# Performance work log

Hardware: AMD Instinct MI355X
Metric: run time of the kernel (lower is better)

Reference implementation:

```python
import jax, jax.numpy as jnp
import numpy as np
from jax import lax

NUM_CHANNELS = 64
DILATION_DEPTH = 9
NUM_REPEAT = 2
KERNEL_SIZE = 3
DILATIONS = [2 ** d for d in range(DILATION_DEPTH)] * NUM_REPEAT  # 18 layers
B, T = 4, 32768


def causal_conv1d(x, w, b, dilation):
    # x: [B, Cin, T], w: [Cout, Cin, K], b: [Cout]
    # left-pad by (K-1)*dilation -> causal, output length T
    pad = (w.shape[-1] - 1) * dilation
    out = lax.conv_general_dilated(
        x, w, window_strides=(1,), padding=[(pad, 0)],
        rhs_dilation=(dilation,), dimension_numbers=("NCH", "OIH", "NCH"))
    return out + b[None, :, None]


def setup_inputs() -> dict:
    key = jax.random.key(0)
    ks = jax.random.split(key, 9)
    L, C = len(DILATIONS), NUM_CHANNELS
    s = 0.05
    return {
        "x": jax.random.normal(ks[0], (B, 1, T), dtype=jnp.float32),
        "in_w": jax.random.normal(ks[1], (C, 1, 1), dtype=jnp.float32) * s,
        "in_b": jax.random.normal(ks[2], (C,), dtype=jnp.float32) * s,
        "hid_w": jax.random.normal(ks[3], (L, 2 * C, C, KERNEL_SIZE), dtype=jnp.float32) * s,
        "hid_b": jax.random.normal(ks[4], (L, 2 * C), dtype=jnp.float32) * s,
        "res_w": jax.random.normal(ks[5], (L, C, C, 1), dtype=jnp.float32) * s,
        "res_b": jax.random.normal(ks[6], (L, C), dtype=jnp.float32) * s,
        "mix_w": jax.random.normal(ks[7], (1, L * C, 1), dtype=jnp.float32) * s,
        "mix_b": jax.random.normal(ks[8], (1,), dtype=jnp.float32) * s,
    }


def reference(x, in_w, in_b, hid_w, hid_b, res_w, res_b, mix_w, mix_b):
    C = NUM_CHANNELS
    out = causal_conv1d(x, in_w, in_b, 1)  # [B, C, T]
    skips = []
    for i, d in enumerate(DILATIONS):
        inp = out
        h = causal_conv1d(inp, hid_w[i], hid_b[i], d)  # [B, 2C, T]
        gated = jnp.tanh(h[:, :C]) * jax.nn.sigmoid(h[:, C:])  # [B, C, T]
        skips.append(gated)
        out = causal_conv1d(gated, res_w[i], res_b[i], 1) + inp
    skip_cat = jnp.concatenate(skips, axis=1)  # [B, L*C, T]
    return causal_conv1d(skip_cat, mix_w, mix_b, 1)  # [B, 1, T]
```

## Files before the change

### kernel.cpp

```cpp
#include <hip/hip_runtime.h>
#include <math.h>

#define T_LEN 32768
#define NB 4
#define NC 64
#define NL 18

typedef __attribute__((ext_vector_type(8))) short s16x8;
typedef __attribute__((ext_vector_type(4))) float f32x4;
#define MFMA_F16 __builtin_amdgcn_mfma_f32_16x16x32_f16

#define BAR_LGKM()                                                   \
    do {                                                             \
        asm volatile("s_waitcnt lgkmcnt(0)" ::: "memory");           \
        __builtin_amdgcn_s_barrier();                                \
        __builtin_amdgcn_sched_barrier(0);                           \
    } while (0)
#define BAR_VM(N)                                                    \
    do {                                                             \
        asm volatile("s_waitcnt vmcnt(%0) lgkmcnt(0)" ::             \
                         "i"(N) : "memory");                         \
        __builtin_amdgcn_s_barrier();                                \
        __builtin_amdgcn_sched_barrier(0);                           \
    } while (0)

__device__ inline unsigned short f2h(float f) {
    _Float16 h = (_Float16)f;
    return __builtin_bit_cast(unsigned short, h);
}
__device__ inline unsigned pack_h2(float a, float b) {
    return (unsigned)f2h(a) | ((unsigned)f2h(b) << 16);
}
__device__ inline float h2f(unsigned short u) {
    return (float)__builtin_bit_cast(_Float16, u);
}
__device__ inline float fast_sigmoid(float x) {
    return __builtin_amdgcn_rcpf(1.f + __expf(-x));
}
__device__ inline float fast_tanh(float x) {
    return 1.f - 2.f * __builtin_amdgcn_rcpf(1.f + __expf(2.f * x));
}

__global__ void prep_kernel(const float* __restrict__ hid_w,
                            const float* __restrict__ res_w,
                            const float* __restrict__ mix_b,
                            unsigned short* __restrict__ Wh,
                            unsigned short* __restrict__ Wr,
                            float* __restrict__ out,
                            float* __restrict__ zerobuf) {
    const int nW1 = NL * 128 * 192;
    const int nW2 = NL * 64 * 64;
    const int nOut = NB * T_LEN;
    const int total = nW1 + nW2 + nOut + 32;
    for (int gid = blockIdx.x * blockDim.x + threadIdx.x; gid < total;
         gid += gridDim.x * blockDim.x) {
        if (gid < nW1) {
            int K = gid % 192;
            int co = (gid / 192) & 127;
            int i = gid / (192 * 128);
            int kt = K >> 6, ci = K & 63;
            Wh[gid] = f2h(hid_w[((i * 128 + co) * 64 + ci) * 3 + kt]);
        } else if (gid < nW1 + nW2) {
            int q = gid - nW1;
            int c = q & 63, co = (q >> 6) & 63, i = q >> 12;
            Wr[q] = f2h(res_w[(i * 64 + co) * 64 + c]);
        } else if (gid < nW1 + nW2 + nOut) {
            out[gid - (nW1 + nW2)] = mix_b[0];
        } else {
            zerobuf[gid - (nW1 + nW2 + nOut)] = 0.f;
        }
    }
}

template <int DIL, bool FIRST, bool LAST>
__launch_bounds__(256, 4)
__global__ void layer_kernel(const unsigned short* __restrict__ actH,
                             unsigned short* __restrict__ outH,
                             const unsigned short* __restrict__ Wh,
                             const float* __restrict__ hb,
                             const unsigned short* __restrict__ Wr,
                             const float* __restrict__ rb,
                             const float* __restrict__ mw,
                             float* __restrict__ skip,
                             const float* __restrict__ zerobuf,
                             const float* __restrict__ x,
                             const float* __restrict__ in_w,
                             const float* __restrict__ in_b) {
    constexpr bool UNI = (DIL < 64);
    constexpr int R = UNI ? (64 + 2 * DIL) : 192;
    constexpr int SLOTS = R * 8;
    constexpr int JMAX = (SLOTS + 255) / 256;
    constexpr int GS_BASE = (UNI ? 128 : 0) * 128;
    constexpr int OUT_BASE = (UNI ? 0 : 64) * 128;
    constexpr int REG = 24576;

    __shared__ uint4 Xs[2 * 1536];
    __shared__ float Sk[256];
    char* lds = (char*)Xs;

    const int tid = threadIdx.x;
    const int w = tid >> 6;
    const int l = tid & 63;
    const int lo = l & 15;
    const int hi = l >> 4;
    const int blk = blockIdx.x;
    const int tile = (blk & 7) * 64 + (blk >> 3);
    const int t0 = tile * 64;
    const int m0 = 16 * w;
    const int c0 = m0 + 4 * hi;

    const float* xB0 = x;

    s16x8 AH[2][6];
    s16x8 AR[2];
#pragma unroll
    for (int mt = 0; mt < 2; mt++) {
        const unsigned short* wp = Wh + (size_t)(m0 + 64 * mt + lo) * 192;
#pragma unroll
        for (int s = 0; s < 6; s++)
            AH[mt][s] = *(const s16x8*)(wp + 32 * s + 8 * hi);
    }
    if (!LAST) {
#pragma unroll
        for (int s = 0; s < 2; s++)
            AR[s] = *(const s16x8*)(Wr + (size_t)(m0 + lo) * 64 + 32 * s + 8 * hi);
    }
    float bA[4], bB[4], rbv[4];
#pragma unroll
    for (int r = 0; r < 4; r++) {
        bA[r] = hb[c0 + r];
        bB[r] = hb[64 + c0 + r];
        rbv[r] = LAST ? 0.f : rb[c0 + r];
    }
    const float4 mw4 = *(const float4*)(mw + c0);

    auto stage_async = [&](int bb, char* X) {
        const unsigned short* aB = actH + (size_t)bb * T_LEN * NC;
#pragma unroll
        for (int jj = 0; jj < JMAX; jj++) {
            int s = (w * JMAX + jj) * 64 + l;
            const void* src;
            if (s >= SLOTS) {
                src = (const void*)(zerobuf + (s & 7) * 4);
            } else {
                int row = s >> 3, ch = s & 7;
                int chunk = ch ^ (row & 7);
                int tg = t0 + (UNI ? (row - 2 * DIL)
                                   : (((row >> 6) - 2) * DIL + (row & 63)));
                src = (tg >= 0)
                          ? (const void*)(aB + (size_t)tg * 64 + chunk * 8)
                          : (const void*)(zerobuf + chunk * 4);
            }
            __builtin_amdgcn_global_load_lds(
                (const __attribute__((address_space(1))) unsigned int*)src,
                (__attribute__((address_space(3))) unsigned int*)(X +
                                                        (w * JMAX + jj) * 1024),
                16, 0, 0);
        }
    };
    auto stage_first = [&](int bb, char* X) {
        const float* xB = xB0 + (size_t)bb * T_LEN;
#pragma unroll
        for (int jj = 0; jj < JMAX; jj++) {
            int p = jj * 256 + tid;
            if (p < SLOTS) {
                int row = p >> 3, ch = p & 7;
                int tg = t0 + row - 2 * DIL;
                unsigned uu[4] = {0u, 0u, 0u, 0u};
                if (tg >= 0) {
                    float a = xB[tg];
#pragma unroll
                    for (int e = 0; e < 4; e++) {
                        float v0 = a * in_w[ch * 8 + 2 * e] + in_b[ch * 8 + 2 * e];
                        float v1 = a * in_w[ch * 8 + 2 * e + 1] + in_b[ch * 8 + 2 * e + 1];
                        uu[e] = pack_h2(v0, v1);
                    }
                }
                int byte = (row * 128 + ch * 16) ^ ((row & 7) << 4);
                *(uint4*)(X + byte) = make_uint4(uu[0], uu[1], uu[2], uu[3]);
            }
        }
    };

    if (FIRST) stage_first(0, lds);
    else       stage_async(0, lds);

#pragma unroll
    for (int j = 0; j < NB; j++) {
        char* X = lds + (j & 1) * REG;
        const int b = j;

        if (j + 1 < NB) {
            if (FIRST) stage_first(j + 1, lds + ((j + 1) & 1) * REG);
            else       stage_async(j + 1, lds + ((j + 1) & 1) * REG);
        }

        if (FIRST)          BAR_LGKM();
        else if (j + 1 < NB) BAR_VM(JMAX);
        else                 BAR_VM(0);

        f32x4 acc[2][4];
#pragma unroll
        for (int mt = 0; mt < 2; mt++)
#pragma unroll
            for (int nt = 0; nt < 4; nt++)
                acc[mt][nt] = (f32x4){0.f, 0.f, 0.f, 0.f};
#pragma unroll
        for (int s = 0; s < 6; s++) {
            const int tap = s >> 1, half = s & 1;
#pragma unroll
            for (int nt = 0; nt < 4; nt++) {
                int t = 16 * nt + lo;
                int row = UNI ? (t + tap * DIL) : (tap * 64 + t);
                int byte = (row * 128 + half * 64 + hi * 16) ^ ((row & 7) << 4);
                s16x8 bx = __builtin_bit_cast(s16x8, *(const uint4*)(X + byte));
                acc[0][nt] = MFMA_F16(AH[0][s], bx, acc[0][nt], 0, 0, 0);
                acc[1][nt] = MFMA_F16(AH[1][s], bx, acc[1][nt], 0, 0, 0);
            }
        }

        float4 inp[4];
        if (!LAST) {
#pragma unroll
            for (int nt = 0; nt < 4; nt++) {
                int t = 16 * nt + lo;
                int rowI = UNI ? (t + 2 * DIL) : (128 + t);
                int byteI = (rowI * 128 + c0 * 2) ^ ((rowI & 7) << 4);
                uint2 hv = *(const uint2*)(X + byteI);
                inp[nt] = make_float4(h2f((unsigned short)(hv.x & 0xffff)),
                                      h2f((unsigned short)(hv.x >> 16)),
                                      h2f((unsigned short)(hv.y & 0xffff)),
                                      h2f((unsigned short)(hv.y >> 16)));
            }
        }

        BAR_LGKM();

#pragma unroll
        for (int nt = 0; nt < 4; nt++) {
            float g[4];
#pragma unroll
            for (int r = 0; r < 4; r++) {
                float hA = acc[0][nt][r] + bA[r];
                float hB = acc[1][nt][r] + bB[r];
                g[r] = fast_tanh(hA) * fast_sigmoid(hB);
            }
            int t = 16 * nt + lo;
            if (!LAST) {
                int byte = (t * 128 + c0 * 2) ^ ((t & 7) << 4);
                *(uint2*)(X + GS_BASE + byte) =
                    make_uint2(pack_h2(g[0], g[1]), pack_h2(g[2], g[3]));
            }
            float sk = g[0] * mw4.x + g[1] * mw4.y + g[2] * mw4.z + g[3] * mw4.w;
            sk += __shfl_xor(sk, 16, 64);
            sk += __shfl_xor(sk, 32, 64);
            if (hi == 0) Sk[w * 64 + nt * 16 + lo] = sk;
        }
        BAR_LGKM();

        if (LAST) {
            if (tid < 64) {
                float s2 = Sk[tid] + Sk[64 + tid] + Sk[128 + tid] + Sk[192 + tid];
                skip[(size_t)b * T_LEN + t0 + tid] += s2;
            }
            BAR_LGKM();
            continue;
        }

        f32x4 acc2[4];
#pragma unroll
        for (int nt = 0; nt < 4; nt++) acc2[nt] = (f32x4){0.f, 0.f, 0.f, 0.f};
#pragma unroll
        for (int s = 0; s < 2; s++) {
#pragma unroll
            for (int nt = 0; nt < 4; nt++) {
                int t = 16 * nt + lo;
                int byte = (t * 128 + s * 64 + hi * 16) ^ ((t & 7) << 4);
                s16x8 bg = __builtin_bit_cast(
                    s16x8, *(const uint4*)(X + GS_BASE + byte));
                acc2[nt] = MFMA_F16(AR[s], bg, acc2[nt], 0, 0, 0);
            }
        }

        char* OutH = X + OUT_BASE;
#pragma unroll
        for (int nt = 0; nt < 4; nt++) {
            int t = 16 * nt + lo;
            float ox = acc2[nt][0] + rbv[0] + inp[nt].x;
            float oy = acc2[nt][1] + rbv[1] + inp[nt].y;
            float oz = acc2[nt][2] + rbv[2] + inp[nt].z;
            float ow = acc2[nt][3] + rbv[3] + inp[nt].w;
            int byteB = (t * 128 + c0 * 2) ^ ((t & 7) << 4);
            *(uint2*)(OutH + byteB) =
                make_uint2(pack_h2(ox, oy), pack_h2(oz, ow));
        }

        if (tid < 64) {
            float s2 = Sk[tid] + Sk[64 + tid] + Sk[128 + tid] + Sk[192 + tid];
            skip[(size_t)b * T_LEN + t0 + tid] += s2;
        }
        BAR_LGKM();

        unsigned short* gH = outH + (size_t)b * T_LEN * NC + (size_t)t0 * 64;
#pragma unroll
        for (int i = 0; i < 2; i++) {
            int u = i * 256 + tid;
            int t = u >> 3, ch = u & 7;
            uint4 v = *(const uint4*)(OutH + t * 128 + ((ch ^ (t & 7)) << 4));
            ((uint4*)gH)[u] = v;
        }
        BAR_LGKM();
    }
}

extern "C" void kernel_launch(void* const* d_in, const int* in_sizes, int n_in,
                              void* d_out, int out_size, void* d_ws, size_t ws_size,
                              hipStream_t stream) {
    const float* x     = (const float*)d_in[0];
    const float* in_w  = (const float*)d_in[1];
    const float* in_b  = (const float*)d_in[2];
    const float* hid_w = (const float*)d_in[3];
    const float* hid_b = (const float*)d_in[4];
    const float* res_w = (const float*)d_in[5];
    const float* res_b = (const float*)d_in[6];
    const float* mix_w = (const float*)d_in[7];
    const float* mix_b = (const float*)d_in[8];
    float* out = (float*)d_out;

    const size_t actN = (size_t)NB * T_LEN * NC;
    unsigned short* H0 = (unsigned short*)d_ws;
    unsigned short* H1 = H0 + actN;
    unsigned short* Wh = H1 + actN;
    unsigned short* Wr = Wh + (size_t)NL * 128 * 192;
    float* zerobuf = (float*)(Wr + (size_t)NL * 64 * 64);

    prep_kernel<<<512, 256, 0, stream>>>(hid_w, res_w, mix_b, Wh, Wr, out,
                                         zerobuf);

    static const int dils[NL] = {1, 2, 4, 8, 16, 32, 64, 128, 256,
                                 1, 2, 4, 8, 16, 32, 64, 128, 256};
    const unsigned short* srcH = H0;
    unsigned short* dstH = H1;

#define LL(D, F, L)                                                           \
    layer_kernel<D, F, L><<<512, 256, 0, stream>>>(                           \
        srcH, dstH, Wh + (size_t)i * 128 * 192, hid_b + (size_t)i * 128,      \
        Wr + (size_t)i * 64 * 64, res_b + (size_t)i * 64,                     \
        mix_w + (size_t)i * 64, out, zerobuf, x, in_w, in_b)

    for (int i = 0; i < NL; i++) {
        if (i == 0) {
            LL(1, true, false);
        } else if (i == NL - 1) {
            LL(256, false, true);
        } else {
            switch (dils[i]) {
                case 1:   LL(1, false, false);   break;
                case 2:   LL(2, false, false);   break;
                case 4:   LL(4, false, false);   break;
                case 8:   LL(8, false, false);   break;
                case 16:  LL(16, false, false);  break;
                case 32:  LL(32, false, false);  break;
                case 64:  LL(64, false, false);  break;
                case 128: LL(128, false, false); break;
                case 256: LL(256, false, false); break;
            }
        }
        const unsigned short* tH = srcH; srcH = dstH; dstH = (unsigned short*)tH;
    }
#undef LL
}
```

Baseline: 349.1 us.

## Fuse all 18 layers into one cooperative persistent kernel with grid sync

Replaces the 18 per-layer kernel launches with a single cooperative mega-kernel that runs every layer body in sequence and uses grid.sync between layers, swapping the ping-pong activation buffers in device code. It is meant to remove per-launch overhead and the kernel-boundary drain between layers. In exchange it depends on cooperative launch support and enough occupancy (checked at runtime, with a fallback to the old launch path). The first and last flags become runtime values, and grid-wide barriers may cost more than launch gaps.

Result: no change. 347.8 us (-0.4%).

```diff
diff --git a/kernel.cpp b/kernel.cpp
--- a/kernel.cpp
+++ b/kernel.cpp
@@ -1,5 +1,8 @@
 #include <hip/hip_runtime.h>
+#include <hip/hip_cooperative_groups.h>
 #include <math.h>
+
+namespace cg = cooperative_groups;
 
 #define T_LEN 32768
 #define NB 4
@@ -51,7 +54,7 @@
     const int nW1 = NL * 128 * 192;
     const int nW2 = NL * 64 * 64;
     const int nOut = NB * T_LEN;
-    const int total = nW1 + nW2 + nOut + 32;
+    const int total = nW1 + nW2 + nOut + 48;
     for (int gid = blockIdx.x * blockDim.x + threadIdx.x; gid < total;
          gid += gridDim.x * blockDim.x) {
         if (gid < nW1) {
@@ -72,20 +75,17 @@
     }
 }
 
-template <int DIL, bool FIRST, bool LAST>
-__launch_bounds__(256, 4)
-__global__ void layer_kernel(const unsigned short* __restrict__ actH,
-                             unsigned short* __restrict__ outH,
-                             const unsigned short* __restrict__ Wh,
-                             const float* __restrict__ hb,
-                             const unsigned short* __restrict__ Wr,
-                             const float* __restrict__ rb,
-                             const float* __restrict__ mw,
-                             float* __restrict__ skip,
-                             const float* __restrict__ zerobuf,
-                             const float* __restrict__ x,
-                             const float* __restrict__ in_w,
-                             const float* __restrict__ in_b) {
+template <int DIL>
+__device__ __forceinline__ void layer_body(
+    const bool first, const bool last,
+    const unsigned short* actH, unsigned short* outH,
+    const unsigned short* Wh, const float* hb,
+    const unsigned short* Wr, const float* rb,
+    const float* mw, float* skip,
+    const float* zerobuf, const float* x,
+    const float* in_w, const float* in_b,
+    char* lds, float* Sk, const int t0)
+{
     constexpr bool UNI = (DIL < 64);
     constexpr int R = UNI ? (64 + 2 * DIL) : 192;
     constexpr int SLOTS = R * 8;
@@ -94,23 +94,14 @@
     constexpr int OUT_BASE = (UNI ? 0 : 64) * 128;
     constexpr int REG = 24576;
 
-    __shared__ uint4 Xs[2 * 1536];
-    __shared__ float Sk[256];
-    char* lds = (char*)Xs;
-
     const int tid = threadIdx.x;
     const int w = tid >> 6;
     const int l = tid & 63;
     const int lo = l & 15;
     const int hi = l >> 4;
-    const int blk = blockIdx.x;
-    const int tile = (blk & 7) * 64 + (blk >> 3);
-    const int t0 = tile * 64;
     const int m0 = 16 * w;
     const int c0 = m0 + 4 * hi;
 
-    const float* xB0 = x;
-
     s16x8 AH[2][6];
     s16x8 AR[2];
 #pragma unroll
@@ -120,7 +111,7 @@
         for (int s = 0; s < 6; s++)
             AH[mt][s] = *(const s16x8*)(wp + 32 * s + 8 * hi);
     }
-    if (!LAST) {
+    if (!(DIL == 256 && last)) {
 #pragma unroll
         for (int s = 0; s < 2; s++)
             AR[s] = *(const s16x8*)(Wr + (size_t)(m0 + lo) * 64 + 32 * s + 8 * hi);
@@ -130,7 +121,7 @@
     for (int r = 0; r < 4; r++) {
         bA[r] = hb[c0 + r];
         bB[r] = hb[64 + c0 + r];
-        rbv[r] = LAST ? 0.f : rb[c0 + r];
+        rbv[r] = (DIL == 256 && last) ? 0.f : rb[c0 + r];
     }
     const float4 mw4 = *(const float4*)(mw + c0);
 
@@ -159,7 +150,7 @@
         }
     };
     auto stage_first = [&](int bb, char* X) {
-        const float* xB = xB0 + (size_t)bb * T_LEN;
+        const float* xB = x + (size_t)bb * T_LEN;
 #pragma unroll
         for (int jj = 0; jj < JMAX; jj++) {
             int p = jj * 256 + tid;
@@ -182,8 +173,8 @@
         }
     };
 
-    if (FIRST) stage_first(0, lds);
-    else       stage_async(0, lds);
+    if (DIL == 1 && first) stage_first(0, lds);
+    else                   stage_async(0, lds);
 
 #pragma unroll
     for (int j = 0; j < NB; j++) {
@@ -191,13 +182,13 @@
         const int b = j;
 
         if (j + 1 < NB) {
-            if (FIRST) stage_first(j + 1, lds + ((j + 1) & 1) * REG);
-            else       stage_async(j + 1, lds + ((j + 1) & 1) * REG);
-        }
-
-        if (FIRST)          BAR_LGKM();
-        else if (j + 1 < NB) BAR_VM(JMAX);
-        else                 BAR_VM(0);
+            if (DIL == 1 && first) stage_first(j + 1, lds + ((j + 1) & 1) * REG);
+            else                   stage_async(j + 1, lds + ((j + 1) & 1) * REG);
+        }
+
+        if (DIL == 1 && first) { BAR_LGKM(); }
+        else if (j + 1 < NB)   { BAR_VM(JMAX); }
+        else                   { BAR_VM(0); }
 
         f32x4 acc[2][4];
 #pragma unroll
@@ -220,7 +211,7 @@
         }
 
         float4 inp[4];
-        if (!LAST) {
+        if (!(DIL == 256 && last)) {
 #pragma unroll
             for (int nt = 0; nt < 4; nt++) {
                 int t = 16 * nt + lo;
@@ -246,7 +237,7 @@
                 g[r] = fast_tanh(hA) * fast_sigmoid(hB);
             }
             int t = 16 * nt + lo;
-            if (!LAST) {
+            if (!(DIL == 256 && last)) {
                 int byte = (t * 128 + c0 * 2) ^ ((t & 7) << 4);
                 *(uint2*)(X + GS_BASE + byte) =
                     make_uint2(pack_h2(g[0], g[1]), pack_h2(g[2], g[3]));
@@ -258,7 +249,7 @@
         }
         BAR_LGKM();
 
-        if (LAST) {
+        if (DIL == 256 && last) {
             if (tid < 64) {
                 float s2 = Sk[tid] + Sk[64 + tid] + Sk[128 + tid] + Sk[192 + tid];
                 skip[(size_t)b * T_LEN + t0 + tid] += s2;
@@ -310,6 +301,67 @@
             ((uint4*)gH)[u] = v;
         }
         BAR_LGKM();
+    }
+}
+
+template <int DIL, bool FIRST, bool LAST>
+__launch_bounds__(256, 4)
+__global__ void layer_kernel(const unsigned short* actH, unsigned short* outH,
+                             const unsigned short* Wh, const float* hb,
+                             const unsigned short* Wr, const float* rb,
+                             const float* mw, float* skip,
+                             const float* zerobuf, const float* x,
+                             const float* in_w, const float* in_b) {
+    __shared__ uint4 Xs[2 * 1536];
+    __shared__ float Sk[256];
+    const int blk = blockIdx.x;
+    const int tile = (blk & 7) * 64 + (blk >> 3);
+    layer_body<DIL>(FIRST, LAST, actH, outH, Wh, hb, Wr, rb, mw, skip,
+                    zerobuf, x, in_w, in_b, (char*)Xs, Sk, tile * 64);
+}
+
+__launch_bounds__(256, 4)
+__global__ void mega_kernel(const unsigned short* H0, unsigned short* H1,
+                            const unsigned short* Wh, const float* hid_b,
+                            const unsigned short* Wr, const float* res_b,
+                            const float* mix_w, float* out,
+                            const float* zerobuf, const float* x,
+                            const float* in_w, const float* in_b)
+{
+    __shared__ uint4 Xs[2 * 1536];
+    __shared__ float Sk[256];
+    char* lds = (char*)Xs;
+
+    cg::grid_group grid = cg::this_grid();
+
+    const int blk = blockIdx.x;
+    const int tile = (blk & 7) * 64 + (blk >> 3);
+    const int t0 = tile * 64;
+
+    const unsigned short* src = H0;
+    unsigned short* dst = H1;
+
+    for (int r = 0; r < 2; r++) {
+#define LBODY(K, D)                                                          \
+        {                                                                    \
+            const int li = r * 9 + K;                                        \
+            const bool first = (D == 1) && (li == 0);                        \
+            const bool last = (D == 256) && (r == 1);                        \
+            layer_body<D>(first, last, src, dst,                             \
+                          Wh + (size_t)li * 128 * 192, hid_b + li * 128,     \
+                          Wr + (size_t)li * 64 * 64, res_b + li * 64,        \
+                          mix_w + li * 64, out, zerobuf, x, in_w, in_b,      \
+                          lds, Sk, t0);                                      \
+            if (!last) {                                                     \
+                grid.sync();                                                 \
+                const unsigned short* tt = src;                              \
+                src = dst;                                                   \
+                dst = (unsigned short*)tt;                                   \
+            }                                                                \
+        }
+        LBODY(0, 1) LBODY(1, 2) LBODY(2, 4) LBODY(3, 8) LBODY(4, 16)
+        LBODY(5, 32) LBODY(6, 64) LBODY(7, 128) LBODY(8, 256)
+#undef LBODY
     }
 }
 
@@ -337,17 +389,42 @@
     prep_kernel<<<512, 256, 0, stream>>>(hid_w, res_w, mix_b, Wh, Wr, out,
                                          zerobuf);
 
-    static const int dils[NL] = {1, 2, 4, 8, 16, 32, 64, 128, 256,
-                                 1, 2, 4, 8, 16, 32, 64, 128, 256};
+    int nbPerCU = 0;
+    hipError_t oe = hipOccupancyMaxActiveBlocksPerMultiprocessor(
+        &nbPerCU, mega_kernel, 256, 0);
+    bool coop = (oe == hipSuccess) && (nbPerCU >= 2);
+
+    if (coop) {
+        const unsigned short* a0 = H0;
+        unsigned short* a1 = H1;
+        const unsigned short* a2 = Wh;
+        const float* a3 = hid_b;
+        const unsigned short* a4 = Wr;
+        const float* a5 = res_b;
+        const float* a6 = mix_w;
+        float* a7 = out;
+        const float* a8 = zerobuf;
+        const float* a9 = x;
+        const float* a10 = in_w;
+        const float* a11 = in_b;
+        void* args[12] = {&a0, &a1, &a2, &a3, &a4, &a5,
+                          &a6, &a7, &a8, &a9, &a10, &a11};
+        hipError_t le = hipLaunchCooperativeKernel(
+            (void*)mega_kernel, dim3(512), dim3(256), args, 0, stream);
+        if (le == hipSuccess) return;
+        coop = false;
+    }
+
     const unsigned short* srcH = H0;
     unsigned short* dstH = H1;
-
 #define LL(D, F, L)                                                           \
     layer_kernel<D, F, L><<<512, 256, 0, stream>>>(                           \
         srcH, dstH, Wh + (size_t)i * 128 * 192, hid_b + (size_t)i * 128,      \
         Wr + (size_t)i * 64 * 64, res_b + (size_t)i * 64,                     \
         mix_w + (size_t)i * 64, out, zerobuf, x, in_w, in_b)
 
+    static const int dils[NL] = {1, 2, 4, 8, 16, 32, 64, 128, 256,
+                                 1, 2, 4, 8, 16, 32, 64, 128, 256};
     for (int i = 0; i < NL; i++) {
         if (i == 0) {
             LL(1, true, false);
```

## Use 512-thread blocks splitting each time tile across two wave groups

Applied to the files above, without the earlier changes.

Doubles the block size so eight waves share each 64-step tile. Each group of four waves handles 32 time steps instead of 64, so each wave issues half as many MFMA tiles and LDS reads. Staging loops, the skip-reduction layout in shared memory and the output store are re-indexed to match. This aims to put more waves on each CU to hide latency, at the cost of each wave pair holding duplicate weight registers and more barrier participants.

New measurement: 448.2 us. +28.4%, slower.

```diff
diff --git a/kernel.cpp b/kernel.cpp
--- a/kernel.cpp
+++ b/kernel.cpp
@@ -51,7 +51,7 @@
     const int nW1 = NL * 128 * 192;
     const int nW2 = NL * 64 * 64;
     const int nOut = NB * T_LEN;
-    const int total = nW1 + nW2 + nOut + 32;
+    const int total = nW1 + nW2 + nOut + 48;
     for (int gid = blockIdx.x * blockDim.x + threadIdx.x; gid < total;
          gid += gridDim.x * blockDim.x) {
         if (gid < nW1) {
@@ -73,7 +73,7 @@
 }
 
 template <int DIL, bool FIRST, bool LAST>
-__launch_bounds__(256, 4)
+__launch_bounds__(512, 4)
 __global__ void layer_kernel(const unsigned short* __restrict__ actH,
                              unsigned short* __restrict__ outH,
                              const unsigned short* __restrict__ Wh,
@@ -89,7 +89,7 @@
     constexpr bool UNI = (DIL < 64);
     constexpr int R = UNI ? (64 + 2 * DIL) : 192;
     constexpr int SLOTS = R * 8;
-    constexpr int JMAX = (SLOTS + 255) / 256;
+    constexpr int JMAX = (SLOTS + 511) / 512;
     constexpr int GS_BASE = (UNI ? 128 : 0) * 128;
     constexpr int OUT_BASE = (UNI ? 0 : 64) * 128;
     constexpr int REG = 24576;
@@ -100,16 +100,17 @@
 
     const int tid = threadIdx.x;
     const int w = tid >> 6;
+    const int wc = w & 3;
+    const int th = w >> 2;
     const int l = tid & 63;
     const int lo = l & 15;
     const int hi = l >> 4;
     const int blk = blockIdx.x;
     const int tile = (blk & 7) * 64 + (blk >> 3);
     const int t0 = tile * 64;
-    const int m0 = 16 * w;
+    const int m0 = 16 * wc;
     const int c0 = m0 + 4 * hi;
-
-    const float* xB0 = x;
+    const int tb = 32 * th;
 
     s16x8 AH[2][6];
     s16x8 AR[2];
@@ -159,10 +160,10 @@
         }
     };
     auto stage_first = [&](int bb, char* X) {
-        const float* xB = xB0 + (size_t)bb * T_LEN;
+        const float* xB = x + (size_t)bb * T_LEN;
 #pragma unroll
         for (int jj = 0; jj < JMAX; jj++) {
-            int p = jj * 256 + tid;
+            int p = jj * 512 + tid;
             if (p < SLOTS) {
                 int row = p >> 3, ch = p & 7;
                 int tg = t0 + row - 2 * DIL;
@@ -195,22 +196,22 @@
             else       stage_async(j + 1, lds + ((j + 1) & 1) * REG);
         }
 
-        if (FIRST)          BAR_LGKM();
-        else if (j + 1 < NB) BAR_VM(JMAX);
-        else                 BAR_VM(0);
-
-        f32x4 acc[2][4];
+        if (FIRST)           { BAR_LGKM(); }
+        else if (j + 1 < NB) { BAR_VM(JMAX); }
+        else                 { BAR_VM(0); }
+
+        f32x4 acc[2][2];
 #pragma unroll
         for (int mt = 0; mt < 2; mt++)
 #pragma unroll
-            for (int nt = 0; nt < 4; nt++)
+            for (int nt = 0; nt < 2; nt++)
                 acc[mt][nt] = (f32x4){0.f, 0.f, 0.f, 0.f};
 #pragma unroll
         for (int s = 0; s < 6; s++) {
             const int tap = s >> 1, half = s & 1;
 #pragma unroll
-            for (int nt = 0; nt < 4; nt++) {
-                int t = 16 * nt + lo;
+            for (int nt = 0; nt < 2; nt++) {
+                int t = tb + 16 * nt + lo;
                 int row = UNI ? (t + tap * DIL) : (tap * 64 + t);
                 int byte = (row * 128 + half * 64 + hi * 16) ^ ((row & 7) << 4);
                 s16x8 bx = __builtin_bit_cast(s16x8, *(const uint4*)(X + byte));
@@ -219,11 +220,11 @@
             }
         }
 
-        float4 inp[4];
+        float4 inp[2];
         if (!LAST) {
 #pragma unroll
-            for (int nt = 0; nt < 4; nt++) {
-                int t = 16 * nt + lo;
+            for (int nt = 0; nt < 2; nt++) {
+                int t = tb + 16 * nt + lo;
                 int rowI = UNI ? (t + 2 * DIL) : (128 + t);
                 int byteI = (rowI * 128 + c0 * 2) ^ ((rowI & 7) << 4);
                 uint2 hv = *(const uint2*)(X + byteI);
@@ -237,7 +238,7 @@
         BAR_LGKM();
 
 #pragma unroll
-        for (int nt = 0; nt < 4; nt++) {
+        for (int nt = 0; nt < 2; nt++) {
             float g[4];
 #pragma unroll
             for (int r = 0; r < 4; r++) {
@@ -245,7 +246,7 @@
                 float hB = acc[1][nt][r] + bB[r];
                 g[r] = fast_tanh(hA) * fast_sigmoid(hB);
             }
-            int t = 16 * nt + lo;
+            int t = tb + 16 * nt + lo;
             if (!LAST) {
                 int byte = (t * 128 + c0 * 2) ^ ((t & 7) << 4);
                 *(uint2*)(X + GS_BASE + byte) =
@@ -254,27 +255,30 @@
             float sk = g[0] * mw4.x + g[1] * mw4.y + g[2] * mw4.z + g[3] * mw4.w;
             sk += __shfl_xor(sk, 16, 64);
             sk += __shfl_xor(sk, 32, 64);
-            if (hi == 0) Sk[w * 64 + nt * 16 + lo] = sk;
+            if (hi == 0) Sk[th * 128 + wc * 32 + 16 * nt + lo] = sk;
         }
         BAR_LGKM();
 
         if (LAST) {
             if (tid < 64) {
-                float s2 = Sk[tid] + Sk[64 + tid] + Sk[128 + tid] + Sk[192 + tid];
-                skip[(size_t)b * T_LEN + t0 + tid] += s2;
+                int t = tid;
+                int base = (t >> 5) * 128 + (t & 31);
+                float s2 = Sk[base] + Sk[base + 32] + Sk[base + 64] +
+                           Sk[base + 96];
+                skip[(size_t)b * T_LEN + t0 + t] += s2;
             }
             BAR_LGKM();
             continue;
         }
 
-        f32x4 acc2[4];
-#pragma unroll
-        for (int nt = 0; nt < 4; nt++) acc2[nt] = (f32x4){0.f, 0.f, 0.f, 0.f};
+        f32x4 acc2[2];
+#pragma unroll
+        for (int nt = 0; nt < 2; nt++) acc2[nt] = (f32x4){0.f, 0.f, 0.f, 0.f};
 #pragma unroll
         for (int s = 0; s < 2; s++) {
 #pragma unroll
-            for (int nt = 0; nt < 4; nt++) {
-                int t = 16 * nt + lo;
+            for (int nt = 0; nt < 2; nt++) {
+                int t = tb + 16 * nt + lo;
                 int byte = (t * 128 + s * 64 + hi * 16) ^ ((t & 7) << 4);
                 s16x8 bg = __builtin_bit_cast(
                     s16x8, *(const uint4*)(X + GS_BASE + byte));
@@ -284,8 +288,8 @@
 
         char* OutH = X + OUT_BASE;
 #pragma unroll
-        for (int nt = 0; nt < 4; nt++) {
-            int t = 16 * nt + lo;
+        for (int nt = 0; nt < 2; nt++) {
+            int t = tb + 16 * nt + lo;
             float ox = acc2[nt][0] + rbv[0] + inp[nt].x;
             float oy = acc2[nt][1] + rbv[1] + inp[nt].y;
             float oz = acc2[nt][2] + rbv[2] + inp[nt].z;
@@ -296,15 +300,16 @@
         }
 
         if (tid < 64) {
-            float s2 = Sk[tid] + Sk[64 + tid] + Sk[128 + tid] + Sk[192 + tid];
-            skip[(size_t)b * T_LEN + t0 + tid] += s2;
+            int t = tid;
+            int base = (t >> 5) * 128 + (t & 31);
+            float s2 = Sk[base] + Sk[base + 32] + Sk[base + 64] + Sk[base + 96];
+            skip[(size_t)b * T_LEN + t0 + t] += s2;
         }
         BAR_LGKM();
 
         unsigned short* gH = outH + (size_t)b * T_LEN * NC + (size_t)t0 * 64;
-#pragma unroll
-        for (int i = 0; i < 2; i++) {
-            int u = i * 256 + tid;
+        {
+            int u = tid;
             int t = u >> 3, ch = u & 7;
             uint4 v = *(const uint4*)(OutH + t * 128 + ((ch ^ (t & 7)) << 4));
             ((uint4*)gH)[u] = v;
@@ -343,7 +348,7 @@
     unsigned short* dstH = H1;
 
 #define LL(D, F, L)                                                           \
-    layer_kernel<D, F, L><<<512, 256, 0, stream>>>(                           \
+    layer_kernel<D, F, L><<<512, 512, 0, stream>>>(                           \
         srcH, dstH, Wh + (size_t)i * 128 * 192, hid_b + (size_t)i * 128,      \
         Wr + (size_t)i * 64 * 64, res_b + (size_t)i * 64,                     \
         mix_w + (size_t)i * 64, out, zerobuf, x, in_w, in_b)
```
